# Optimization experiments

Hardware: AMD Instinct MI355X
Metric: run time of the kernel (lower is better)

The kernel has to match this reference:

```python
import jax, jax.numpy as jnp
import numpy as np

H = 128          # controller hidden size
NCELL = 8        # memory cells
CS = 8           # cell size
R = 1            # read heads
L = 16           # stacked DNC layers
E = 15           # embedding size
NCLS = 30
NUMFRI = 5
NN_IN = H + R * CS                   # 136, controller input width (layers > 0)
XI = R * CS + 3 * CS + 5 * R + 3     # 40, interface vector size
CLIP = 20.0
EPS = 1e-6
B, T = 128, 64
NOT_EYE = 1.0 - np.eye(NCELL, dtype=np.float32)


def setup_inputs() -> dict:
    key = jax.random.key(0)
    ks = iter(jax.random.split(key, 40))
    n = lambda shape, s=0.05: jax.random.normal(next(ks), shape, dtype=jnp.float32) * s
    return {
        "x": jax.random.randint(next(ks), (B, T), 0, NCLS, dtype=jnp.int32),
        "f": n((B, H * NUMFRI), 1.0),
        "embed": n((NCLS + 3, E), 1.0),
        # LSTM controller: [layer, sublayer(2), 4H, in] with in padded to NN_IN
        "W_ih": n((L, 2, 4 * H, NN_IN)),
        "W_hh": n((L, 2, 4 * H, H)),
        "b_ih": n((L, 2, 4 * H)),
        "b_hh": n((L, 2, 4 * H)),
        "W_if": n((XI, H)),            # memory interface
        "b_if": n((XI,)),
        "W_out": n((H, NN_IN)),        # final DNC output linear
        "b_out": n((H,)),
        "W_fri": n((H, H * NUMFRI)),
        "b_fri": n((H,)),
        "W_c1": n((H, 2 * H)),
        "b_c1": n((H,)),
        "W_c2": n((NCLS, H)),
        "b_c2": n((NCLS,)),
    }


def lstm_cell(x, h, c, wih, whh, bih, bhh):
    g = x @ wih.T + h @ whh.T + bih + bhh
    i, f, gg, o = jnp.split(g, 4, axis=-1)  # torch gate order i,f,g,o
    c2 = jax.nn.sigmoid(f) * c + jax.nn.sigmoid(i) * jnp.tanh(gg)
    h2 = jax.nn.sigmoid(o) * jnp.tanh(c2)
    return h2, c2


def content_weight(mem, keys, strengths):
    # cosine similarity between keys [b,h,cs] and memory rows [b,m,cs]
    mn = mem / (jnp.linalg.norm(mem, axis=2, keepdims=True) + EPS)
    kn = keys / (jnp.linalg.norm(keys, axis=2, keepdims=True) + EPS)
    sim = jnp.einsum('bhc,bmc->bhm', kn, mn)
    return jax.nn.softmax(sim * strengths[:, :, None], axis=2)


def allocate(usage):
    u = EPS + (1.0 - EPS) * usage
    phi = jnp.argsort(u, axis=1)          # free list (ascending usage)
    su = jnp.take_along_axis(u, phi, axis=1)
    shifted = jnp.cumprod(jnp.concatenate([jnp.ones_like(su[:, :1]), su], axis=1), axis=1)[:, :-1]
    sa = (1.0 - su) * shifted
    phi_rev = jnp.argsort(phi, axis=1)    # inverse permutation
    return jnp.take_along_axis(sa, phi_rev, axis=1)[:, None, :]   # [b,1,m]


def memory_step(xi, mstate):
    mem, link, prec, rw, ww, usage = mstate
    b = xi.shape[0]
    rk = jnp.tanh(xi[:, :R * CS].reshape(b, R, CS))
    rs = jax.nn.softplus(xi[:, R * CS:R * CS + R])
    wk = jnp.tanh(xi[:, R * CS + R:R * CS + R + CS].reshape(b, 1, CS))
    ws = jax.nn.softplus(xi[:, R * CS + R + CS:R * CS + R + CS + 1])
    er = jax.nn.sigmoid(xi[:, R * CS + R + CS + 1:R * CS + R + 2 * CS + 1].reshape(b, 1, CS))
    wv = jnp.tanh(xi[:, R * CS + R + 2 * CS + 1:R * CS + R + 3 * CS + 1].reshape(b, 1, CS))
    fg = jax.nn.sigmoid(xi[:, R * CS + R + 3 * CS + 1:R * CS + 2 * R + 3 * CS + 1])
    ag = jax.nn.sigmoid(xi[:, R * CS + 2 * R + 3 * CS + 1:R * CS + 2 * R + 3 * CS + 2])
    wg = jax.nn.sigmoid(xi[:, R * CS + 2 * R + 3 * CS + 2:R * CS + 2 * R + 3 * CS + 3])
    modes = jax.nn.softmax(xi[:, R * CS + 2 * R + 3 * CS + 3:].reshape(b, R, 3), axis=-1)
    # --- write ---
    usage = usage + (1 - usage) * (1 - jnp.prod(1 - ww, axis=1))
    psi = jnp.prod(1 - fg[:, :, None] * rw, axis=1)
    usage = usage * psi
    wcw = content_weight(mem, wk, ws)                  # [b,1,m]
    alloc = allocate(usage)
    a3 = ag[:, :, None]; g3 = wg[:, :, None]
    ww = g3 * (a3 * alloc + (1 - a3) * wcw)            # [b,1,m]
    reset = jnp.prod(1 - ww[:, :, :, None] * er[:, :, None, :], axis=1)  # [b,m,cs]
    mem = mem * reset + jnp.einsum('bhm,bhc->bmc', ww, wv)
    ww_i = ww[:, :, :, None]; ww_j = ww[:, :, None, :]
    link = (1 - ww_i - ww_j) * link + ww_i * prec[:, :, None, :]
    link = link * NOT_EYE[None, None]
    prec = (1 - jnp.sum(ww, axis=2, keepdims=True)) * prec + ww
    # --- read ---
    cw = content_weight(mem, rk, rs)                   # [b,r,m]
    fwdw = jnp.einsum('bhij,brj->brhi', link, rw)      # forward weightings
    bwdw = jnp.einsum('bri,bhij->brhj', rw, link)      # backward weightings
    rw = (modes[:, :, 2:3] * cw
          + jnp.sum(modes[:, :, 1:2][:, :, :, None] * fwdw, axis=2)
          + jnp.sum(modes[:, :, 0:1][:, :, :, None] * bwdw, axis=2))
    read_vecs = jnp.einsum('brm,bmc->brc', rw, mem).reshape(b, R * CS)
    return read_vecs, (mem, link, prec, rw, ww, usage)


def _forward(x, f, embed, W_ih, W_hh, b_ih, b_hh, W_if, b_if, W_out, b_out,
             W_fri, b_fri, W_c1, b_c1, W_c2, b_c2):
    b = x.shape[0]
    emb = embed[x]                                     # [b,t,E]
    carry0 = (jnp.zeros((L, 2, b, H), jnp.float32), jnp.zeros((L, 2, b, H), jnp.float32),
              jnp.zeros((b, NCELL, CS), jnp.float32), jnp.zeros((b, 1, NCELL, NCELL), jnp.float32),
              jnp.zeros((b, 1, NCELL), jnp.float32), jnp.zeros((b, R, NCELL), jnp.float32),
              jnp.zeros((b, 1, NCELL), jnp.float32), jnp.zeros((b, NCELL), jnp.float32))

    def step(carry, x_t):
        h, c, mem, link, prec, rw, ww, usage = carry
        inp = x_t   # layer-0 sees [x_t, zero initial read] (reset_experience=True); zeros come from padding
        hs, cs = [], []
        for l in range(L):
            xin = jnp.pad(inp, ((0, 0), (0, NN_IN - inp.shape[1])))
            h0, c0 = lstm_cell(xin, h[l, 0], c[l, 0], W_ih[l, 0], W_hh[l, 0], b_ih[l, 0], b_hh[l, 0])
            xin1 = jnp.pad(h0, ((0, 0), (0, NN_IN - H)))
            h1, c1 = lstm_cell(xin1, h[l, 1], c[l, 1], W_ih[l, 1], W_hh[l, 1], b_ih[l, 1], b_hh[l, 1])
            hs.append(jnp.stack([h0, h1])); cs.append(jnp.stack([c0, c1]))
            out = jnp.clip(h1, -CLIP, CLIP)
            xi = out @ W_if.T + b_if
            read_vecs, (mem, link, prec, rw, ww, usage) = memory_step(xi, (mem, link, prec, rw, ww, usage))
            inp = jnp.concatenate([out, read_vecs], axis=1)   # [b, 136] -> next layer
        y = inp @ W_out.T + b_out
        return (jnp.stack(hs), jnp.stack(cs), mem, link, prec, rw, ww, usage), y

    _, ys = jax.lax.scan(step, carry0, emb.transpose(1, 0, 2))
    z = ys[-1]                                         # encoder output = last timestep [b,H]
    f_out = jax.nn.relu(f @ W_fri.T + b_fri)
    hcat = jnp.concatenate([z, f_out], axis=1)         # [b,2H]
    h1 = jax.nn.relu(hcat @ W_c1.T + b_c1)
    return h1 @ W_c2.T + b_c2                          # [b, n_class]


def reference(x, f, embed, W_ih, W_hh, b_ih, b_hh, W_if, b_if, W_out, b_out,
              W_fri, b_fri, W_c1, b_c1, W_c2, b_c2):
    return _forward(x, f, embed, W_ih, W_hh, b_ih, b_hh, W_if, b_if, W_out, b_out,
                    W_fri, b_fri, W_c1, b_c1, W_c2, b_c2)
```

## Files before the change

### kernel.cpp

```cpp
#include <hip/hip_runtime.h>
#include <stdint.h>

#define LNUM 16
#define H 128
#define TT 64
#define NCLSN 30
#define EPSF 1e-6f

typedef _Float16 half2v __attribute__((ext_vector_type(2)));

__device__ inline float fdot2(uint32_t a, uint32_t b, float c) {
  return __builtin_amdgcn_fdot2(__builtin_bit_cast(half2v, a),
                                __builtin_bit_cast(half2v, b), c, false);
}
__device__ inline float dot8(uint4 w, uint4 xv, float a) {
  a = fdot2(w.x, xv.x, a); a = fdot2(w.y, xv.y, a);
  a = fdot2(w.z, xv.z, a); a = fdot2(w.w, xv.w, a);
  return a;
}
__device__ __forceinline__ float rcpf(float x) { return __builtin_amdgcn_rcpf(x); }
__device__ inline float sigf(float x) { return rcpf(1.0f + __expf(-x)); }
__device__ __forceinline__ float tanh_fast(float x) {
  float xc = fminf(fmaxf(x, -15.f), 15.f);
  float e = __expf(2.f * xc);
  return (e - 1.f) * rcpf(e + 1.f);
}
__device__ __forceinline__ float softplus_fast(float x) {
  return fmaxf(x, 0.f) + __logf(1.f + __expf(-fabsf(x)));
}
__device__ inline uint32_t packh2(float a, float b) {
  half2v h; h.x = (_Float16)a; h.y = (_Float16)b;
  return __builtin_bit_cast(uint32_t, h);
}
__device__ inline uint16_t f16bits(float a) {
  _Float16 h = (_Float16)a;
  return __builtin_bit_cast(uint16_t, h);
}
__device__ __forceinline__ void gl_lds16(const uint4* g, uint4* l) {
  __builtin_amdgcn_global_load_lds(
      (const __attribute__((address_space(1))) void*)g,
      (__attribute__((address_space(3))) void*)l, 16, 0, 0);
}
__device__ __forceinline__ void bar_lgkm() {
  asm volatile("s_waitcnt lgkmcnt(0)\ns_barrier" ::: "memory");
}

__global__ void prepA(const float* __restrict__ W_ih, const float* __restrict__ W_hh,
                      uint4* __restrict__ WB) {
  int idx = blockIdx.x * 256 + threadIdx.x;
  int lc = idx / 16896;
  int r  = idx % 16896;
  int row, kq;
  if (r < 16384) {
    int q = r >> 11;
    int rem = r & 2047;
    int g = rem >> 9;
    int gt = rem & 511;
    int j = gt >> 2, s = gt & 3;
    kq = s + 4 * q;
    row = g * 128 + j;
  } else {
    int r2 = r - 16384;
    int g = r2 >> 7, j = r2 & 127;
    kq = 32; row = g * 128 + j;
  }
  bool zero = ((lc & 1) && kq == 16);
  uint32_t p[4];
#pragma unroll
  for (int i2 = 0; i2 < 4; i2++) {
    float w0 = 0.f, w1 = 0.f;
    if (!zero) {
      int k0 = 8 * kq + 2 * i2;
      w0 = (k0 < 136) ? W_ih[((size_t)lc * 512 + row) * 136 + k0]
                      : W_hh[((size_t)lc * 512 + row) * 128 + (k0 - 136)];
      w1 = (k0 + 1 < 136) ? W_ih[((size_t)lc * 512 + row) * 136 + k0 + 1]
                          : W_hh[((size_t)lc * 512 + row) * 128 + (k0 + 1 - 136)];
    }
    p[i2] = packh2(w0, w1);
  }
  uint4 v; v.x = p[0]; v.y = p[1]; v.z = p[2]; v.w = p[3];
  WB[idx] = v;
}

__global__ void prepB(const float* __restrict__ b_ih, const float* __restrict__ b_hh,
                      const float* __restrict__ W_if, const float* __restrict__ W_fri,
                      const float* __restrict__ W_c1, const float* __restrict__ W_c2,
                      float* __restrict__ bias_comb, uint32_t* __restrict__ Wif16,
                      float* __restrict__ WfriT, float* __restrict__ Wc1T,
                      float* __restrict__ Wc2T) {
  int idx = blockIdx.x * 256 + threadIdx.x;
  if (idx < 16384) { bias_comb[idx] = b_ih[idx] + b_hh[idx]; return; }
  idx -= 16384;
  if (idx < 2560)  {
    int j = idx / 64, k2 = idx % 64;
    Wif16[idx] = packh2(W_if[j * 128 + 2 * k2], W_if[j * 128 + 2 * k2 + 1]);
    return;
  }
  idx -= 2560;
  if (idx < 81920) { int k = idx / 128, j = idx % 128; WfriT[idx] = W_fri[j * 640 + k]; return; }
  idx -= 81920;
  if (idx < 32768) { int k = idx / 128, j = idx % 128; Wc1T[idx]  = W_c1[j * 256 + k]; return; }
  idx -= 32768;
  if (idx < 3840)  { int k = idx / 30,  j = idx % 30;  Wc2T[idx]  = W_c2[j * 128 + k]; return; }
}

__device__ __forceinline__ void memstep_par(
    int m, const float* __restrict__ xi,
    float (&mm)[8], float (&lkr)[8],
    float& u, float& p, float& r, float& w,
    float (&rv)[8]) {
  float rk[8], wk[8], er[8], wv[8];
#pragma unroll
  for (int c = 0; c < 8; c++) {
    rk[c] = tanh_fast(xi[c]);
    wk[c] = tanh_fast(xi[9 + c]);
    er[c] = sigf(xi[18 + c]);
    wv[c] = tanh_fast(xi[26 + c]);
  }
  float rs  = softplus_fast(xi[8]);
  float wsd = softplus_fast(xi[17]);
  float fg  = sigf(xi[34]), ag = sigf(xi[35]), wg = sigf(xi[36]);
  float l0 = xi[37], l1 = xi[38], l2 = xi[39];
  float lmx = fmaxf(l0, fmaxf(l1, l2));
  float eb = __expf(l0 - lmx), ef = __expf(l1 - lmx), ec = __expf(l2 - lmx);
  float minv = rcpf(eb + ef + ec);
  float mode_b = eb * minv, mode_f = ef * minv, mode_c = ec * minv;

  u = u + (1.f - u) * w;
  u *= (1.f - fg * r);

  float kn2 = 0.f, mn2 = 0.f, dp = 0.f;
#pragma unroll
  for (int c = 0; c < 8; c++) { kn2 += wk[c]*wk[c]; mn2 += mm[c]*mm[c]; dp += wk[c]*mm[c]; }
  float sim = dp * rcpf((sqrtf(kn2) + EPSF) * (sqrtf(mn2) + EPSF)) * wsd;
  float mx = sim;
  mx = fmaxf(mx, __shfl_xor(mx, 1));
  mx = fmaxf(mx, __shfl_xor(mx, 2));
  mx = fmaxf(mx, __shfl_xor(mx, 4));
  float e = __expf(sim - mx);
  float se = e;
  se += __shfl_xor(se, 1); se += __shfl_xor(se, 2); se += __shfl_xor(se, 4);
  float wcw = e * rcpf(se);

  float up = EPSF + (1.f - EPSF) * u;
  float prod = 1.f;
#pragma unroll
  for (int n = 0; n < 8; n++) {
    float un = __shfl(up, n);
    bool before = (un < up) || (un == up && n < m);
    prod *= ((n != m) && before) ? un : 1.f;
  }
  float alloc = (1.f - up) * prod;
  float wn = wg * (ag * alloc + (1.f - ag) * wcw);
  float sw = wn;
  sw += __shfl_xor(sw, 1); sw += __shfl_xor(sw, 2); sw += __shfl_xor(sw, 4);

#pragma unroll
  for (int c = 0; c < 8; c++)
    mm[c] = mm[c] * (1.f - wn * er[c]) + wn * wv[c];

  float wnv[8], pvv[8];
#pragma unroll
  for (int n = 0; n < 8; n++) { wnv[n] = __shfl(wn, n); pvv[n] = __shfl(p, n); }
#pragma unroll
  for (int jj = 0; jj < 8; jj++)
    lkr[jj] = (jj == m) ? 0.f : ((1.f - wn - wnv[jj]) * lkr[jj] + wn * pvv[jj]);
  p = (1.f - sw) * p + wn;

  float rn2 = 0.f; mn2 = 0.f; dp = 0.f;
#pragma unroll
  for (int c = 0; c < 8; c++) { rn2 += rk[c]*rk[c]; mn2 += mm[c]*mm[c]; dp += rk[c]*mm[c]; }
  float sim2 = dp * rcpf((sqrtf(rn2) + EPSF) * (sqrtf(mn2) + EPSF)) * rs;
  float mx2 = sim2;
  mx2 = fmaxf(mx2, __shfl_xor(mx2, 1));
  mx2 = fmaxf(mx2, __shfl_xor(mx2, 2));
  mx2 = fmaxf(mx2, __shfl_xor(mx2, 4));
  float e2 = __expf(sim2 - mx2);
  float se2 = e2;
  se2 += __shfl_xor(se2, 1); se2 += __shfl_xor(se2, 2); se2 += __shfl_xor(se2, 4);
  float cw = e2 * rcpf(se2);

  float rv8[8];
#pragma unroll
  for (int n = 0; n < 8; n++) rv8[n] = __shfl(r, n);
  float fwd = 0.f;
#pragma unroll
  for (int jj = 0; jj < 8; jj++) fwd += lkr[jj] * rv8[jj];
  float bw[8];
#pragma unroll
  for (int jj = 0; jj < 8; jj++) bw[jj] = r * lkr[jj];
#pragma unroll
  for (int jj = 0; jj < 8; jj++) {
    bw[jj] += __shfl_xor(bw[jj], 1);
    bw[jj] += __shfl_xor(bw[jj], 2);
    bw[jj] += __shfl_xor(bw[jj], 4);
  }
  bool s1 = (m & 1) != 0, s2 = (m & 2) != 0, s4 = (m & 4) != 0;
  float t0 = s1 ? bw[1] : bw[0];
  float t1 = s1 ? bw[3] : bw[2];
  float t2 = s1 ? bw[5] : bw[4];
  float t3 = s1 ? bw[7] : bw[6];
  float q0 = s2 ? t1 : t0;
  float q1 = s2 ? t3 : t2;
  float bwd = s4 ? q1 : q0;

  float rn = mode_c * cw + mode_f * fwd + mode_b * bwd;

#pragma unroll
  for (int c = 0; c < 8; c++) rv[c] = rn * mm[c];
#pragma unroll
  for (int c = 0; c < 8; c++) {
    rv[c] += __shfl_xor(rv[c], 1);
    rv[c] += __shfl_xor(rv[c], 2);
    rv[c] += __shfl_xor(rv[c], 4);
  }
  r = rn; w = wn;
}

__device__ __forceinline__ void aux_work(
    int lane, bool write_inp,
    const uint4 (&wreg)[16], const float* __restrict__ b_if,
    const uint4* __restrict__ outhu4, float* __restrict__ xi_lds,
    uint4* __restrict__ inpu4,
    float (&mm)[8], float (&lkr)[8],
    float& u, float& p, float& r, float& w,
    float (&rv)[8]) {
  if (lane < 40) {
    float acc0 = 0.f, acc1 = 0.f;
#pragma unroll
    for (int q = 0; q < 8; q++) {
      acc0 = dot8(wreg[2 * q],     outhu4[2 * q],     acc0);
      acc1 = dot8(wreg[2 * q + 1], outhu4[2 * q + 1], acc1);
    }
    xi_lds[lane] = acc0 + acc1 + b_if[lane];
  }
  asm volatile("s_waitcnt lgkmcnt(0)" ::: "memory");
  __builtin_amdgcn_sched_barrier(0);
  __builtin_amdgcn_wave_barrier();
  if (lane < 8) {
    memstep_par(lane, xi_lds, mm, lkr, u, p, r, w, rv);
    if (write_inp && lane == 0) {
      uint4 pv4;
      pv4.x = packh2(rv[0], rv[1]); pv4.y = packh2(rv[2], rv[3]);
      pv4.z = packh2(rv[4], rv[5]); pv4.w = packh2(rv[6], rv[7]);
      inpu4[16] = pv4;
    }
  }
}

#define STAGE(lcX, qX, bbX)                                                    \
  do {                                                                         \
    const uint4* sp_ = WB + (size_t)(lcX) * 16896 + (size_t)(qX) * 2048 + tid; \
    uint4* dp_ = myslab + (size_t)(bbX) * 256;                                 \
    gl_lds16(sp_,        dp_);                                                 \
    gl_lds16(sp_ + 512,  dp_ + 64);                                            \
    gl_lds16(sp_ + 1024, dp_ + 128);                                           \
    gl_lds16(sp_ + 1536, dp_ + 192);                                           \
  } while (0)

__global__ __launch_bounds__(576) void dnc_main(
    const int* __restrict__ x, const float* __restrict__ embed,
    const uint4* __restrict__ WB, const float* __restrict__ bias_comb,
    const uint32_t* __restrict__ Wif16, const float* __restrict__ b_if,
    const float* __restrict__ W_out, const float* __restrict__ b_out,
    float* __restrict__ y_buf) {
  __shared__ __align__(16) uint16_t hst[32 * 128];
  __shared__ float c_st[32 * 128];
  __shared__ float emb_lds[495];
  __shared__ __align__(16) uint32_t inp16[17 * 4];
  __shared__ __align__(16) uint16_t outh16[128];
  __shared__ float inp_f32[128];
  __shared__ float xi_lds[40];
  __shared__ float rv_f32[8];
  __shared__ __align__(16) uint4 sbuf[8 * 4 * 256];

  uint4* inpu4 = (uint4*)inp16;
  uint4* hstu4 = (uint4*)hst;
  uint4* outhu4 = (uint4*)outh16;
  uint16_t* inpu16 = (uint16_t*)inp16;

  const int tid = threadIdx.x;
  const int b0 = blockIdx.x;
  const int ln = tid & 63;
  uint4* myslab = sbuf + (size_t)(tid >> 6) * 1024;

  float mm[8] = {0.f,0.f,0.f,0.f,0.f,0.f,0.f,0.f};
  float lkr[8] = {0.f,0.f,0.f,0.f,0.f,0.f,0.f,0.f};
  float p_u = 0.f, p_p = 0.f, p_r = 0.f, p_w = 0.f;
  float rvout[8];

  uint4 wreg[16];
  if (tid >= 512 && (tid & 63) < 40) {
    const uint4* wr = (const uint4*)(Wif16 + (tid & 63) * 64);
#pragma unroll
    for (int q = 0; q < 16; q++) wreg[q] = wr[q];
  }

  for (int i = tid; i < 32 * 128; i += 576) { hst[i] = 0; c_st[i] = 0.f; }
  for (int i = tid; i < 495; i += 576) emb_lds[i] = embed[i];
  __syncthreads();
  if (tid < 17) {
    int q = tid;
    int ix = x[b0 * TT + 0];
    uint32_t p0, p1, p2, p3;
    {
      int k0 = 8 * q;
      float e0 = (k0 < 15) ? emb_lds[ix * 15 + k0] : 0.f;
      float e1 = (k0 + 1 < 15) ? emb_lds[ix * 15 + k0 + 1] : 0.f;
      float e2 = (k0 + 2 < 15) ? emb_lds[ix * 15 + k0 + 2] : 0.f;
      float e3 = (k0 + 3 < 15) ? emb_lds[ix * 15 + k0 + 3] : 0.f;
      float e4 = (k0 + 4 < 15) ? emb_lds[ix * 15 + k0 + 4] : 0.f;
      float e5 = (k0 + 5 < 15) ? emb_lds[ix * 15 + k0 + 5] : 0.f;
      float e6 = (k0 + 6 < 15) ? emb_lds[ix * 15 + k0 + 6] : 0.f;
      float e7 = (k0 + 7 < 15) ? emb_lds[ix * 15 + k0 + 7] : 0.f;
      p0 = packh2(e0, e1); p1 = packh2(e2, e3); p2 = packh2(e4, e5); p3 = packh2(e6, e7);
    }
    uint4 v; v.x = p0; v.y = p1; v.z = p2; v.w = p3;
    inpu4[q] = v;
  }
  if (tid < 512) { STAGE(0, 0, 0); STAGE(0, 1, 1); STAGE(0, 2, 2); }
  __syncthreads();

  for (int t = 0; t < TT; ++t) {
    for (int l = 0; l < LNUM; ++l) {
      const int lc0 = l * 2, lc1 = l * 2 + 1;
      const int nlc0 = (l == 15) ? 0 : lc0 + 2;
      const int j = tid >> 2, s = tid & 3;
      float aA0 = 0.f, aA1 = 0.f, aA2 = 0.f, aA3 = 0.f;
      uint4 wd0 = {}, wd1 = {}, wd2 = {}, wd3 = {};
      float bA0 = 0.f, bA1 = 0.f, bA2 = 0.f, bA3 = 0.f;

      if (tid < 512) {
        uint4 wt0 = {}, wt1 = {}, wt2 = {}, wt3 = {};
        if (s == 0) {
          const uint4* wt = WB + (size_t)lc0 * 16896 + 16384 + j;
          wt0 = wt[0]; wt1 = wt[128]; wt2 = wt[256]; wt3 = wt[384];
        }
        if (s == 0) {
          const float* bb = bias_comb + lc0 * 512 + j;
          bA0 = bb[0]; bA1 = bb[128]; bA2 = bb[256]; bA3 = bb[384];
        }
#pragma unroll
        for (int q = 0; q < 8; q++) {
          if (q < 5) STAGE(lc0, q + 3, (q + 3) & 3);
          else       STAGE(lc1, q - 5, (q + 3) & 3);
          asm volatile("s_waitcnt vmcnt(12)" ::: "memory");
          __builtin_amdgcn_sched_barrier(0);
          const uint4* wb = myslab + (size_t)(q & 3) * 256 + ln;
          uint4 w0 = wb[0], w1 = wb[64], w2 = wb[128], w3 = wb[192];
          int kq = s + 4 * q;
          bool defer = (s == 0) && (q == 4);
          int kqe = defer ? 0 : kq;
          const uint4* xp = (kqe < 17) ? (inpu4 + kqe)
                                       : (hstu4 + lc0 * 16 + (kqe - 17));
          uint4 xv0 = *xp;
          if (defer) { wd0 = w0; wd1 = w1; wd2 = w2; wd3 = w3; }
          else {
            aA0 = dot8(w0, xv0, aA0);
            aA1 = dot8(w1, xv0, aA1);
            aA2 = dot8(w2, xv0, aA2);
            aA3 = dot8(w3, xv0, aA3);
          }
        }
        if (s == 0) {
          uint4 xv0 = hstu4[lc0 * 16 + 15];
          aA0 = dot8(wt0, xv0, aA0);
          aA1 = dot8(wt1, xv0, aA1);
          aA2 = dot8(wt2, xv0, aA2);
          aA3 = dot8(wt3, xv0, aA3);
        }
      } else if (t > 0 || l > 0) {
        const int lane = tid - 512;
        aux_work(lane, (l != 0), wreg, b_if, outhu4, xi_lds,
                 inpu4, mm, lkr, p_u, p_p, p_r, p_w, rvout);
      }
      bar_lgkm();

      if (tid < 512) {
        if (s == 0) {
          uint4 xr0 = inpu4[16];
          aA0 = dot8(wd0, xr0, aA0);
          aA1 = dot8(wd1, xr0, aA1);
          aA2 = dot8(wd2, xr0, aA2);
          aA3 = dot8(wd3, xr0, aA3);
        }
        aA0 += __shfl_xor(aA0, 1); aA0 += __shfl_xor(aA0, 2);
        aA1 += __shfl_xor(aA1, 1); aA1 += __shfl_xor(aA1, 2);
        aA2 += __shfl_xor(aA2, 1); aA2 += __shfl_xor(aA2, 2);
        aA3 += __shfl_xor(aA3, 1); aA3 += __shfl_xor(aA3, 2);
        if (s == 0) {
          float gi = aA0 + bA0, gf = aA1 + bA1, gg = aA2 + bA2, go = aA3 + bA3;
          int ci = lc0 * 128 + j;
          float c2 = sigf(gf) * c_st[ci] + sigf(gi) * tanh_fast(gg);
          c_st[ci] = c2;
          hst[ci] = f16bits(sigf(go) * tanh_fast(c2));
        }
      }
      bar_lgkm();

      if (tid < 512) {
        float cA0 = 0.f, cA1 = 0.f, cA2 = 0.f, cA3 = 0.f;
        uint4 wt0 = {}, wt1 = {}, wt2 = {}, wt3 = {};
        float bC0 = 0.f, bC1 = 0.f, bC2 = 0.f, bC3 = 0.f;
        if (s == 0) {
          const uint4* wt = WB + (size_t)lc1 * 16896 + 16384 + j;
          wt0 = wt[0]; wt1 = wt[128]; wt2 = wt[256]; wt3 = wt[384];
          const float* bb = bias_comb + lc1 * 512 + j;
          bC0 = bb[0]; bC1 = bb[128]; bC2 = bb[256]; bC3 = bb[384];
        }
#pragma unroll
        for (int q = 0; q < 8; q++) {
          if (q < 5) STAGE(lc1, q + 3, (q + 3) & 3);
          else       STAGE(nlc0, q - 5, (q + 3) & 3);
          asm volatile("s_waitcnt vmcnt(12)" ::: "memory");
          __builtin_amdgcn_sched_barrier(0);
          const uint4* wb = myslab + (size_t)(q & 3) * 256 + ln;
          uint4 w0 = wb[0], w1 = wb[64], w2 = wb[128], w3 = wb[192];
          int kq = s + 4 * q;
          const uint4* xp = (kq < 17) ? (hstu4 + lc0 * 16 + kq)
                                      : (hstu4 + lc1 * 16 + (kq - 17));
          uint4 xv0 = *xp;
          cA0 = dot8(w0, xv0, cA0);
          cA1 = dot8(w1, xv0, cA1);
          cA2 = dot8(w2, xv0, cA2);
          cA3 = dot8(w3, xv0, cA3);
        }
        if (s == 0) {
          uint4 xv0 = hstu4[lc1 * 16 + 15];
          cA0 = dot8(wt0, xv0, cA0);
          cA1 = dot8(wt1, xv0, cA1);
          cA2 = dot8(wt2, xv0, cA2);
          cA3 = dot8(wt3, xv0, cA3);
        }
        cA0 += __shfl_xor(cA0, 1); cA0 += __shfl_xor(cA0, 2);
        cA1 += __shfl_xor(cA1, 1); cA1 += __shfl_xor(cA1, 2);
        cA2 += __shfl_xor(cA2, 1); cA2 += __shfl_xor(cA2, 2);
        cA3 += __shfl_xor(cA3, 1); cA3 += __shfl_xor(cA3, 2);
        if (s == 0) {
          float gi = cA0 + bC0, gf = cA1 + bC1, gg = cA2 + bC2, go = cA3 + bC3;
          int ci = lc1 * 128 + j;
          float c2 = sigf(gf) * c_st[ci] + sigf(gi) * tanh_fast(gg);
          c_st[ci] = c2;
          float h2 = sigf(go) * tanh_fast(c2);
          hst[ci] = f16bits(h2);
          inp_f32[j] = h2;
          outh16[j] = f16bits(h2);
          if (l != 15) inpu16[j] = f16bits(h2);
        }
      } else {
        const int lane = tid - 512;
        if (l == 15 && t < 63 && lane < 17) {
          int q = lane;
          int ix = x[b0 * TT + t + 1];
          uint32_t p0, p1, p2, p3;
          {
            int k0 = 8 * q;
            float e0 = (k0 < 15) ? emb_lds[ix * 15 + k0] : 0.f;
            float e1 = (k0 + 1 < 15) ? emb_lds[ix * 15 + k0 + 1] : 0.f;
            float e2 = (k0 + 2 < 15) ? emb_lds[ix * 15 + k0 + 2] : 0.f;
            float e3 = (k0 + 3 < 15) ? emb_lds[ix * 15 + k0 + 3] : 0.f;
            float e4 = (k0 + 4 < 15) ? emb_lds[ix * 15 + k0 + 4] : 0.f;
            float e5 = (k0 + 5 < 15) ? emb_lds[ix * 15 + k0 + 5] : 0.f;
            float e6 = (k0 + 6 < 15) ? emb_lds[ix * 15 + k0 + 6] : 0.f;
            float e7 = (k0 + 7 < 15) ? emb_lds[ix * 15 + k0 + 7] : 0.f;
            p0 = packh2(e0, e1); p1 = packh2(e2, e3); p2 = packh2(e4, e5); p3 = packh2(e6, e7);
          }
          uint4 v; v.x = p0; v.y = p1; v.z = p2; v.w = p3;
          inpu4[q] = v;
        }
      }
      bar_lgkm();
    }
  }

  if (tid >= 512) {
    const int lane = tid - 512;
    aux_work(lane, false, wreg, b_if, outhu4, xi_lds,
             inpu4, mm, lkr, p_u, p_p, p_r, p_w, rvout);
    if (lane == 0) {
#pragma unroll
      for (int c = 0; c < 8; c++) rv_f32[c] = rvout[c];
    }
  }
  __syncthreads();
  if (tid < 128) {
    int i = tid;
    float a = b_out[i];
    for (int k = 0; k < 128; ++k) a += inp_f32[k] * W_out[i * 136 + k];
    for (int k = 0; k < 8; ++k)   a += rv_f32[k] * W_out[i * 136 + 128 + k];
    y_buf[b0 * H + i] = a;
  }
}

__global__ void head_kernel(const float* __restrict__ y_buf, const float* __restrict__ f,
                            const float* __restrict__ WfriT, const float* __restrict__ b_fri,
                            const float* __restrict__ Wc1T, const float* __restrict__ b_c1,
                            const float* __restrict__ Wc2T, const float* __restrict__ b_c2,
                            float* __restrict__ out) {
  __shared__ float fl[640], yl[128], fo[128], h1l[128];
  int b = blockIdx.x, j = threadIdx.x;
  for (int i = j; i < 640; i += 128) fl[i] = f[b * 640 + i];
  yl[j] = y_buf[b * 128 + j];
  __syncthreads();
  float a = b_fri[j];
  for (int k = 0; k < 640; ++k) a += fl[k] * WfriT[k * 128 + j];
  fo[j] = fmaxf(a, 0.f);
  __syncthreads();
  float a2 = b_c1[j];
  for (int k = 0; k < 128; ++k) a2 += yl[k] * Wc1T[k * 128 + j];
  for (int k = 0; k < 128; ++k) a2 += fo[k] * Wc1T[(128 + k) * 128 + j];
  h1l[j] = fmaxf(a2, 0.f);
  __syncthreads();
  if (j < NCLSN) {
    float a3 = b_c2[j];
    for (int k = 0; k < 128; ++k) a3 += h1l[k] * Wc2T[k * NCLSN + j];
    out[b * NCLSN + j] = a3;
  }
}

extern "C" void kernel_launch(void* const* d_in, const int* in_sizes, int n_in,
                              void* d_out, int out_size, void* d_ws, size_t ws_size,
                              hipStream_t stream) {
  const int*   x     = (const int*)d_in[0];
  const float* f     = (const float*)d_in[1];
  const float* embed = (const float*)d_in[2];
  const float* W_ih  = (const float*)d_in[3];
  const float* W_hh  = (const float*)d_in[4];
  const float* b_ih  = (const float*)d_in[5];
  const float* b_hh  = (const float*)d_in[6];
  const float* W_if  = (const float*)d_in[7];
  const float* b_if  = (const float*)d_in[8];
  const float* W_out = (const float*)d_in[9];
  const float* b_out = (const float*)d_in[10];
  const float* W_fri = (const float*)d_in[11];
  const float* b_fri = (const float*)d_in[12];
  const float* W_c1  = (const float*)d_in[13];
  const float* b_c1  = (const float*)d_in[14];
  const float* W_c2  = (const float*)d_in[15];
  const float* b_c2  = (const float*)d_in[16];

  uint8_t* ws = (uint8_t*)d_ws;
  uint4* WB        = (uint4*)(ws + 0);
  float* bias_comb = (float*)(ws + 8650752);
  uint32_t* Wif16  = (uint32_t*)(ws + 8716288);
  float* WfriT     = (float*)(ws + 8726528);
  float* Wc1T      = (float*)(ws + 9054208);
  float* Wc2T      = (float*)(ws + 9185280);
  float* y_buf     = (float*)(ws + 9200640);
  float* out       = (float*)d_out;

  prepA<<<2112, 256, 0, stream>>>(W_ih, W_hh, WB);
  prepB<<<537, 256, 0, stream>>>(b_ih, b_hh, W_if, W_fri, W_c1, W_c2,
                                 bias_comb, Wif16, WfriT, Wc1T, Wc2T);
  dnc_main<<<128, 576, 0, stream>>>(x, embed, WB, bias_comb, Wif16, b_if,
                                    W_out, b_out, y_buf);
  head_kernel<<<128, 128, 0, stream>>>(y_buf, f, WfriT, b_fri, Wc1T, b_c1,
                                       Wc2T, b_c2, out);
}
```

Before: 10.03 ms.

## Repartition LSTM gate matvec across 16 waves with row-pair split and deeper weight ring

Raises the main recurrent kernel from 576 to 1024 threads. Gate rows are now split across 14 gate waves, with two lanes per row streaming weights through an 8-slot LDS ring. A 15th wave reads its last 64 rows straight from global, and the 16th wave runs the memory/interface work. Biases are folded into the packed weights as an extra column dotted with a constant one, and the interface weights move from registers to LDS. The gate nonlinearity is computed by 128 threads from a shared gates buffer. This adds an extra barrier per sublayer in exchange for more parallelism and fewer serial dot products per thread.

```diff
diff --git a/kernel.cpp b/kernel.cpp
--- a/kernel.cpp
+++ b/kernel.cpp
@@ -2,10 +2,10 @@
 #include <stdint.h>
 
 #define LNUM 16
-#define H 128
 #define TT 64
 #define NCLSN 30
 #define EPSF 1e-6f
+#define NBUF 8
 
 typedef _Float16 half2v __attribute__((ext_vector_type(2)));
 
@@ -45,52 +45,76 @@
   asm volatile("s_waitcnt lgkmcnt(0)\ns_barrier" ::: "memory");
 }
 
-__global__ void prepA(const float* __restrict__ W_ih, const float* __restrict__ W_hh,
-                      uint4* __restrict__ WB) {
+__global__ void prepWR(const float* __restrict__ W_ih, const float* __restrict__ W_hh,
+                       const float* __restrict__ b_ih, const float* __restrict__ b_hh,
+                       uint4* __restrict__ WR) {
   int idx = blockIdx.x * 256 + threadIdx.x;
-  int lc = idx / 16896;
-  int r  = idx % 16896;
-  int row, kq;
-  if (r < 16384) {
-    int q = r >> 11;
-    int rem = r & 2047;
-    int g = rem >> 9;
-    int gt = rem & 511;
-    int j = gt >> 2, s = gt & 3;
-    kq = s + 4 * q;
-    row = g * 128 + j;
+  if (idx >= 487424) return;
+  int tid = idx % 896;
+  int rem = idx / 896;
+  int i = rem % 17;
+  int lc = rem / 17;
+  int r = tid >> 1, s = tid & 1;
+  uint32_t p0 = 0, p1 = 0, p2 = 0, p3 = 0;
+  if (s == 1 && i == 16) {
+    float b = b_ih[(size_t)lc * 512 + r] + b_hh[(size_t)lc * 512 + r];
+    p0 = packh2(b, 0.f);
   } else {
-    int r2 = r - 16384;
-    int g = r2 >> 7, j = r2 & 127;
-    kq = 32; row = g * 128 + j;
-  }
-  bool zero = ((lc & 1) && kq == 16);
-  uint32_t p[4];
-#pragma unroll
-  for (int i2 = 0; i2 < 4; i2++) {
-    float w0 = 0.f, w1 = 0.f;
+    int c = s ? 17 + i : i;
+    bool zero = ((lc & 1) != 0) && (c == 16);
     if (!zero) {
-      int k0 = 8 * kq + 2 * i2;
-      w0 = (k0 < 136) ? W_ih[((size_t)lc * 512 + row) * 136 + k0]
-                      : W_hh[((size_t)lc * 512 + row) * 128 + (k0 - 136)];
-      w1 = (k0 + 1 < 136) ? W_ih[((size_t)lc * 512 + row) * 136 + k0 + 1]
-                          : W_hh[((size_t)lc * 512 + row) * 128 + (k0 + 1 - 136)];
-    }
-    p[i2] = packh2(w0, w1);
-  }
-  uint4 v; v.x = p[0]; v.y = p[1]; v.z = p[2]; v.w = p[3];
-  WB[idx] = v;
-}
-
-__global__ void prepB(const float* __restrict__ b_ih, const float* __restrict__ b_hh,
-                      const float* __restrict__ W_if, const float* __restrict__ W_fri,
+      float w[8];
+#pragma unroll
+      for (int e = 0; e < 8; e++) {
+        int k = 8 * c + e;
+        w[e] = (k < 136) ? W_ih[((size_t)lc * 512 + r) * 136 + k]
+                         : W_hh[((size_t)lc * 512 + r) * 128 + (k - 136)];
+      }
+      p0 = packh2(w[0], w[1]); p1 = packh2(w[2], w[3]);
+      p2 = packh2(w[4], w[5]); p3 = packh2(w[6], w[7]);
+    }
+  }
+  uint4 v; v.x = p0; v.y = p1; v.z = p2; v.w = p3;
+  WR[idx] = v;
+}
+
+__global__ void prepWC(const float* __restrict__ W_ih, const float* __restrict__ W_hh,
+                       const float* __restrict__ b_ih, const float* __restrict__ b_hh,
+                       uint4* __restrict__ WC) {
+  int idx = blockIdx.x * 256 + threadIdx.x;
+  if (idx >= 69632) return;
+  int k = idx % 64;
+  int rem = idx / 64;
+  int c = rem % 34;
+  int lc = rem / 34;
+  int r = 448 + k;
+  uint32_t p0 = 0, p1 = 0, p2 = 0, p3 = 0;
+  if (c == 33) {
+    float b = b_ih[(size_t)lc * 512 + r] + b_hh[(size_t)lc * 512 + r];
+    p0 = packh2(b, 0.f);
+  } else {
+    bool zero = ((lc & 1) != 0) && (c == 16);
+    if (!zero) {
+      float w[8];
+#pragma unroll
+      for (int e = 0; e < 8; e++) {
+        int kk = 8 * c + e;
+        w[e] = (kk < 136) ? W_ih[((size_t)lc * 512 + r) * 136 + kk]
+                          : W_hh[((size_t)lc * 512 + r) * 128 + (kk - 136)];
+      }
+      p0 = packh2(w[0], w[1]); p1 = packh2(w[2], w[3]);
+      p2 = packh2(w[4], w[5]); p3 = packh2(w[6], w[7]);
+    }
+  }
+  uint4 v; v.x = p0; v.y = p1; v.z = p2; v.w = p3;
+  WC[idx] = v;
+}
+
+__global__ void prepB(const float* __restrict__ W_if, const float* __restrict__ W_fri,
                       const float* __restrict__ W_c1, const float* __restrict__ W_c2,
-                      float* __restrict__ bias_comb, uint32_t* __restrict__ Wif16,
-                      float* __restrict__ WfriT, float* __restrict__ Wc1T,
-                      float* __restrict__ Wc2T) {
+                      uint32_t* __restrict__ Wif16, float* __restrict__ WfriT,
+                      float* __restrict__ Wc1T, float* __restrict__ Wc2T) {
   int idx = blockIdx.x * 256 + threadIdx.x;
-  if (idx < 16384) { bias_comb[idx] = b_ih[idx] + b_hh[idx]; return; }
-  idx -= 16384;
   if (idx < 2560)  {
     int j = idx / 64, k2 = idx % 64;
     Wif16[idx] = packh2(W_if[j * 128 + 2 * k2], W_if[j * 128 + 2 * k2 + 1]);
@@ -218,8 +242,8 @@
 }
 
 __device__ __forceinline__ void aux_work(
-    int lane, bool write_inp,
-    const uint4 (&wreg)[16], const float* __restrict__ b_if,
+    int lane, bool write_inp, float bifr,
+    const uint4* __restrict__ wifu4,
     const uint4* __restrict__ outhu4, float* __restrict__ xi_lds,
     uint4* __restrict__ inpu4,
     float (&mm)[8], float (&lkr)[8],
@@ -227,12 +251,13 @@
     float (&rv)[8]) {
   if (lane < 40) {
     float acc0 = 0.f, acc1 = 0.f;
+    const uint4* wr = wifu4 + lane * 16;
 #pragma unroll
     for (int q = 0; q < 8; q++) {
-      acc0 = dot8(wreg[2 * q],     outhu4[2 * q],     acc0);
-      acc1 = dot8(wreg[2 * q + 1], outhu4[2 * q + 1], acc1);
-    }
-    xi_lds[lane] = acc0 + acc1 + b_if[lane];
+      acc0 = dot8(wr[2 * q],     outhu4[2 * q],     acc0);
+      acc1 = dot8(wr[2 * q + 1], outhu4[2 * q + 1], acc1);
+    }
+    xi_lds[lane] = acc0 + acc1 + bifr;
   }
   asm volatile("s_waitcnt lgkmcnt(0)" ::: "memory");
   __builtin_amdgcn_sched_barrier(0);
@@ -248,235 +273,209 @@
   }
 }
 
-#define STAGE(lcX, qX, bbX)                                                    \
-  do {                                                                         \
-    const uint4* sp_ = WB + (size_t)(lcX) * 16896 + (size_t)(qX) * 2048 + tid; \
-    uint4* dp_ = myslab + (size_t)(bbX) * 256;                                 \
-    gl_lds16(sp_,        dp_);                                                 \
-    gl_lds16(sp_ + 512,  dp_ + 64);                                            \
-    gl_lds16(sp_ + 1024, dp_ + 128);                                           \
-    gl_lds16(sp_ + 1536, dp_ + 192);                                           \
-  } while (0)
-
-__global__ __launch_bounds__(576) void dnc_main(
+__global__ __launch_bounds__(1024) void dnc_main(
     const int* __restrict__ x, const float* __restrict__ embed,
-    const uint4* __restrict__ WB, const float* __restrict__ bias_comb,
+    const uint4* __restrict__ WR, const uint4* __restrict__ WC,
     const uint32_t* __restrict__ Wif16, const float* __restrict__ b_if,
     const float* __restrict__ W_out, const float* __restrict__ b_out,
     float* __restrict__ y_buf) {
   __shared__ __align__(16) uint16_t hst[32 * 128];
   __shared__ float c_st[32 * 128];
+  __shared__ float gates_lds[512];
+  __shared__ __align__(16) uint32_t wif_lds[2560];
   __shared__ float emb_lds[495];
   __shared__ __align__(16) uint32_t inp16[17 * 4];
   __shared__ __align__(16) uint16_t outh16[128];
   __shared__ float inp_f32[128];
   __shared__ float xi_lds[40];
   __shared__ float rv_f32[8];
-  __shared__ __align__(16) uint4 sbuf[8 * 4 * 256];
+  __shared__ __align__(16) uint4 one1v;
+  __shared__ __align__(16) uint4 sbuf[14 * NBUF * 64];
 
   uint4* inpu4 = (uint4*)inp16;
   uint4* hstu4 = (uint4*)hst;
   uint4* outhu4 = (uint4*)outh16;
   uint16_t* inpu16 = (uint16_t*)inp16;
+  const uint4* wifu4 = (const uint4*)wif_lds;
 
   const int tid = threadIdx.x;
   const int b0 = blockIdx.x;
-  const int ln = tid & 63;
-  uint4* myslab = sbuf + (size_t)(tid >> 6) * 1024;
+  const int wave = tid >> 6, lane = tid & 63;
+  const bool isGW  = (wave < 14);
+  const bool isW14 = (wave == 14);
+  const int r = tid >> 1, s = tid & 1;
+  uint4* myslab = sbuf + (size_t)wave * (NBUF * 64);
 
   float mm[8] = {0.f,0.f,0.f,0.f,0.f,0.f,0.f,0.f};
   float lkr[8] = {0.f,0.f,0.f,0.f,0.f,0.f,0.f,0.f};
   float p_u = 0.f, p_p = 0.f, p_r = 0.f, p_w = 0.f;
   float rvout[8];
-
-  uint4 wreg[16];
-  if (tid >= 512 && (tid & 63) < 40) {
-    const uint4* wr = (const uint4*)(Wif16 + (tid & 63) * 64);
-#pragma unroll
-    for (int q = 0; q < 16; q++) wreg[q] = wr[q];
-  }
-
-  for (int i = tid; i < 32 * 128; i += 576) { hst[i] = 0; c_st[i] = 0.f; }
-  for (int i = tid; i < 495; i += 576) emb_lds[i] = embed[i];
+  float bifr = 0.f;
+  if (wave == 15 && lane < 40) bifr = b_if[lane];
+
+  for (int i = tid; i < 32 * 128; i += 1024) { hst[i] = 0; c_st[i] = 0.f; }
+  for (int i = tid; i < 2560; i += 1024) wif_lds[i] = Wif16[i];
+  for (int i = tid; i < 495; i += 1024) emb_lds[i] = embed[i];
+  if (tid == 0) { uint4 v; v.x = packh2(1.f, 0.f); v.y = 0; v.z = 0; v.w = 0; one1v = v; }
   __syncthreads();
   if (tid < 17) {
     int q = tid;
     int ix = x[b0 * TT + 0];
-    uint32_t p0, p1, p2, p3;
-    {
-      int k0 = 8 * q;
-      float e0 = (k0 < 15) ? emb_lds[ix * 15 + k0] : 0.f;
-      float e1 = (k0 + 1 < 15) ? emb_lds[ix * 15 + k0 + 1] : 0.f;
-      float e2 = (k0 + 2 < 15) ? emb_lds[ix * 15 + k0 + 2] : 0.f;
-      float e3 = (k0 + 3 < 15) ? emb_lds[ix * 15 + k0 + 3] : 0.f;
-      float e4 = (k0 + 4 < 15) ? emb_lds[ix * 15 + k0 + 4] : 0.f;
-      float e5 = (k0 + 5 < 15) ? emb_lds[ix * 15 + k0 + 5] : 0.f;
-      float e6 = (k0 + 6 < 15) ? emb_lds[ix * 15 + k0 + 6] : 0.f;
-      float e7 = (k0 + 7 < 15) ? emb_lds[ix * 15 + k0 + 7] : 0.f;
-      p0 = packh2(e0, e1); p1 = packh2(e2, e3); p2 = packh2(e4, e5); p3 = packh2(e6, e7);
-    }
-    uint4 v; v.x = p0; v.y = p1; v.z = p2; v.w = p3;
+    uint32_t e[8];
+#pragma unroll
+    for (int e2 = 0; e2 < 8; e2++) {
+      int k0 = 8 * q + e2;
+      ((float*)e)[e2] = (k0 < 15) ? emb_lds[ix * 15 + k0] : 0.f;
+    }
+    float* ef = (float*)e;
+    uint4 v;
+    v.x = packh2(ef[0], ef[1]); v.y = packh2(ef[2], ef[3]);
+    v.z = packh2(ef[4], ef[5]); v.w = packh2(ef[6], ef[7]);
     inpu4[q] = v;
   }
-  if (tid < 512) { STAGE(0, 0, 0); STAGE(0, 1, 1); STAGE(0, 2, 2); }
   __syncthreads();
+
+  int base = 0;
+  if (isGW) {
+#pragma unroll
+    for (int p5 = 0; p5 < 7; p5++)
+      gl_lds16(WR + (size_t)p5 * 896 + tid, myslab + (size_t)p5 * 64);
+  }
 
   for (int t = 0; t < TT; ++t) {
     for (int l = 0; l < LNUM; ++l) {
       const int lc0 = l * 2, lc1 = l * 2 + 1;
       const int nlc0 = (l == 15) ? 0 : lc0 + 2;
-      const int j = tid >> 2, s = tid & 3;
-      float aA0 = 0.f, aA1 = 0.f, aA2 = 0.f, aA3 = 0.f;
-      uint4 wd0 = {}, wd1 = {}, wd2 = {}, wd3 = {};
-      float bA0 = 0.f, bA1 = 0.f, bA2 = 0.f, bA3 = 0.f;
-
-      if (tid < 512) {
-        uint4 wt0 = {}, wt1 = {}, wt2 = {}, wt3 = {};
-        if (s == 0) {
-          const uint4* wt = WB + (size_t)lc0 * 16896 + 16384 + j;
-          wt0 = wt[0]; wt1 = wt[128]; wt2 = wt[256]; wt3 = wt[384];
+      float acc = 0.f;
+      uint4 wd = {};
+
+      if (isGW) {
+#pragma unroll
+        for (int q = 0; q < 17; q++) {
+          asm volatile("s_waitcnt vmcnt(6)" ::: "memory");
+          __builtin_amdgcn_sched_barrier(0);
+          uint4 w = myslab[(size_t)((base + q) & 7) * 64 + lane];
+          uint4 xv;
+          if (s == 0) xv = (q < 16) ? inpu4[q] : inpu4[16];
+          else        xv = (q < 16) ? hstu4[lc0 * 16 + q] : one1v;
+          if (s == 0 && q == 16) wd = w;
+          else acc = dot8(w, xv, acc);
+          const int pp = q + 7;
+          const uint4* src = (pp <= 16)
+              ? WR + ((size_t)lc0 * 17 + pp) * 896 + tid
+              : WR + ((size_t)lc1 * 17 + (pp - 17)) * 896 + tid;
+          gl_lds16(src, myslab + (size_t)((base + pp) & 7) * 64);
         }
-        if (s == 0) {
-          const float* bb = bias_comb + lc0 * 512 + j;
-          bA0 = bb[0]; bA1 = bb[128]; bA2 = bb[256]; bA3 = bb[384];
-        }
-#pragma unroll
-        for (int q = 0; q < 8; q++) {
-          if (q < 5) STAGE(lc0, q + 3, (q + 3) & 3);
-          else       STAGE(lc1, q - 5, (q + 3) & 3);
-          asm volatile("s_waitcnt vmcnt(12)" ::: "memory");
-          __builtin_amdgcn_sched_barrier(0);
-          const uint4* wb = myslab + (size_t)(q & 3) * 256 + ln;
-          uint4 w0 = wb[0], w1 = wb[64], w2 = wb[128], w3 = wb[192];
-          int kq = s + 4 * q;
-          bool defer = (s == 0) && (q == 4);
-          int kqe = defer ? 0 : kq;
-          const uint4* xp = (kqe < 17) ? (inpu4 + kqe)
-                                       : (hstu4 + lc0 * 16 + (kqe - 17));
-          uint4 xv0 = *xp;
-          if (defer) { wd0 = w0; wd1 = w1; wd2 = w2; wd3 = w3; }
-          else {
-            aA0 = dot8(w0, xv0, aA0);
-            aA1 = dot8(w1, xv0, aA1);
-            aA2 = dot8(w2, xv0, aA2);
-            aA3 = dot8(w3, xv0, aA3);
-          }
-        }
-        if (s == 0) {
-          uint4 xv0 = hstu4[lc0 * 16 + 15];
-          aA0 = dot8(wt0, xv0, aA0);
-          aA1 = dot8(wt1, xv0, aA1);
-          aA2 = dot8(wt2, xv0, aA2);
-          aA3 = dot8(wt3, xv0, aA3);
-        }
-      } else if (t > 0 || l > 0) {
-        const int lane = tid - 512;
-        aux_work(lane, (l != 0), wreg, b_if, outhu4, xi_lds,
-                 inpu4, mm, lkr, p_u, p_p, p_r, p_w, rvout);
-      }
-      bar_lgkm();
-
-      if (tid < 512) {
-        if (s == 0) {
-          uint4 xr0 = inpu4[16];
-          aA0 = dot8(wd0, xr0, aA0);
-          aA1 = dot8(wd1, xr0, aA1);
-          aA2 = dot8(wd2, xr0, aA2);
-          aA3 = dot8(wd3, xr0, aA3);
-        }
-        aA0 += __shfl_xor(aA0, 1); aA0 += __shfl_xor(aA0, 2);
-        aA1 += __shfl_xor(aA1, 1); aA1 += __shfl_xor(aA1, 2);
-        aA2 += __shfl_xor(aA2, 1); aA2 += __shfl_xor(aA2, 2);
-        aA3 += __shfl_xor(aA3, 1); aA3 += __shfl_xor(aA3, 2);
-        if (s == 0) {
-          float gi = aA0 + bA0, gf = aA1 + bA1, gg = aA2 + bA2, go = aA3 + bA3;
-          int ci = lc0 * 128 + j;
-          float c2 = sigf(gf) * c_st[ci] + sigf(gi) * tanh_fast(gg);
-          c_st[ci] = c2;
-          hst[ci] = f16bits(sigf(go) * tanh_fast(c2));
-        }
-      }
-      bar_lgkm();
-
-      if (tid < 512) {
-        float cA0 = 0.f, cA1 = 0.f, cA2 = 0.f, cA3 = 0.f;
-        uint4 wt0 = {}, wt1 = {}, wt2 = {}, wt3 = {};
-        float bC0 = 0.f, bC1 = 0.f, bC2 = 0.f, bC3 = 0.f;
-        if (s == 0) {
-          const uint4* wt = WB + (size_t)lc1 * 16896 + 16384 + j;
-          wt0 = wt[0]; wt1 = wt[128]; wt2 = wt[256]; wt3 = wt[384];
-          const float* bb = bias_comb + lc1 * 512 + j;
-          bC0 = bb[0]; bC1 = bb[128]; bC2 = bb[256]; bC3 = bb[384];
-        }
-#pragma unroll
-        for (int q = 0; q < 8; q++) {
-          if (q < 5) STAGE(lc1, q + 3, (q + 3) & 3);
-          else       STAGE(nlc0, q - 5, (q + 3) & 3);
-          asm volatile("s_waitcnt vmcnt(12)" ::: "memory");
-          __builtin_amdgcn_sched_barrier(0);
-          const uint4* wb = myslab + (size_t)(q & 3) * 256 + ln;
-          uint4 w0 = wb[0], w1 = wb[64], w2 = wb[128], w3 = wb[192];
-          int kq = s + 4 * q;
-          const uint4* xp = (kq < 17) ? (hstu4 + lc0 * 16 + kq)
-                                      : (hstu4 + lc1 * 16 + (kq - 17));
-          uint4 xv0 = *xp;
-          cA0 = dot8(w0, xv0, cA0);
-          cA1 = dot8(w1, xv0, cA1);
-          cA2 = dot8(w2, xv0, cA2);
-          cA3 = dot8(w3, xv0, cA3);
-        }
-        if (s == 0) {
-          uint4 xv0 = hstu4[lc1 * 16 + 15];
-          cA0 = dot8(wt0, xv0, cA0);
-          cA1 = dot8(wt1, xv0, cA1);
-          cA2 = dot8(wt2, xv0, cA2);
-          cA3 = dot8(wt3, xv0, cA3);
-        }
-        cA0 += __shfl_xor(cA0, 1); cA0 += __shfl_xor(cA0, 2);
-        cA1 += __shfl_xor(cA1, 1); cA1 += __shfl_xor(cA1, 2);
-        cA2 += __shfl_xor(cA2, 1); cA2 += __shfl_xor(cA2, 2);
-        cA3 += __shfl_xor(cA3, 1); cA3 += __shfl_xor(cA3, 2);
-        if (s == 0) {
-          float gi = cA0 + bC0, gf = cA1 + bC1, gg = cA2 + bC2, go = cA3 + bC3;
-          int ci = lc1 * 128 + j;
-          float c2 = sigf(gf) * c_st[ci] + sigf(gi) * tanh_fast(gg);
-          c_st[ci] = c2;
-          float h2 = sigf(go) * tanh_fast(c2);
-          hst[ci] = f16bits(h2);
-          inp_f32[j] = h2;
-          outh16[j] = f16bits(h2);
-          if (l != 15) inpu16[j] = f16bits(h2);
+      } else if (isW14) {
+        const uint4* wc = WC + (size_t)lc0 * 34 * 64 + lane;
+#pragma unroll
+        for (int c = 0; c < 34; c++) {
+          uint4 w = wc[c * 64];
+          if (c == 16) { wd = w; continue; }
+          uint4 xv;
+          if (c < 16)      xv = inpu4[c];
+          else if (c < 33) xv = hstu4[lc0 * 16 + (c - 17)];
+          else             xv = one1v;
+          acc = dot8(w, xv, acc);
         }
       } else {
-        const int lane = tid - 512;
+        if (t > 0 || l > 0)
+          aux_work(lane, (l != 0), bifr, wifu4, outhu4,
+                   xi_lds, inpu4, mm, lkr, p_u, p_p, p_r, p_w, rvout);
+      }
+      base = (base + 17) & 7;
+      bar_lgkm();
+
+      if (isGW) {
+        if (s == 0) acc = dot8(wd, inpu4[16], acc);
+        acc += __shfl_xor(acc, 1);
+        if (s == 0) gates_lds[r] = acc;
+      } else if (isW14) {
+        acc = dot8(wd, inpu4[16], acc);
+        gates_lds[448 + lane] = acc;
+      }
+      bar_lgkm();
+
+      if (tid < 128) {
+        float gi = gates_lds[tid], gf = gates_lds[128 + tid];
+        float gg = gates_lds[256 + tid], go = gates_lds[384 + tid];
+        int ci = lc0 * 128 + tid;
+        float c2 = sigf(gf) * c_st[ci] + sigf(gi) * tanh_fast(gg);
+        c_st[ci] = c2;
+        hst[ci] = f16bits(sigf(go) * tanh_fast(c2));
+      }
+      bar_lgkm();
+
+      float cacc = 0.f;
+      if (isGW) {
+#pragma unroll
+        for (int q = 0; q < 17; q++) {
+          asm volatile("s_waitcnt vmcnt(6)" ::: "memory");
+          __builtin_amdgcn_sched_barrier(0);
+          uint4 w = myslab[(size_t)((base + q) & 7) * 64 + lane];
+          uint4 xv;
+          if (s == 0) xv = (q < 16) ? hstu4[lc0 * 16 + q] : one1v;
+          else        xv = (q < 16) ? hstu4[lc1 * 16 + q] : one1v;
+          cacc = dot8(w, xv, cacc);
+          const int pp = q + 7;
+          const uint4* src = (pp <= 16)
+              ? WR + ((size_t)lc1 * 17 + pp) * 896 + tid
+              : WR + ((size_t)nlc0 * 17 + (pp - 17)) * 896 + tid;
+          gl_lds16(src, myslab + (size_t)((base + pp) & 7) * 64);
+        }
+        cacc += __shfl_xor(cacc, 1);
+        if (s == 0) gates_lds[r] = cacc;
+      } else if (isW14) {
+        const uint4* wc = WC + (size_t)lc1 * 34 * 64 + lane;
+#pragma unroll
+        for (int c = 0; c < 34; c++) {
+          uint4 w = wc[c * 64];
+          uint4 xv;
+          if (c < 16)       xv = hstu4[lc0 * 16 + c];
+          else if (c == 16) xv = one1v;
+          else if (c < 33)  xv = hstu4[lc1 * 16 + (c - 17)];
+          else              xv = one1v;
+          cacc = dot8(w, xv, cacc);
+        }
+        gates_lds[448 + lane] = cacc;
+      } else {
         if (l == 15 && t < 63 && lane < 17) {
           int q = lane;
           int ix = x[b0 * TT + t + 1];
-          uint32_t p0, p1, p2, p3;
-          {
-            int k0 = 8 * q;
-            float e0 = (k0 < 15) ? emb_lds[ix * 15 + k0] : 0.f;
-            float e1 = (k0 + 1 < 15) ? emb_lds[ix * 15 + k0 + 1] : 0.f;
-            float e2 = (k0 + 2 < 15) ? emb_lds[ix * 15 + k0 + 2] : 0.f;
-            float e3 = (k0 + 3 < 15) ? emb_lds[ix * 15 + k0 + 3] : 0.f;
-            float e4 = (k0 + 4 < 15) ? emb_lds[ix * 15 + k0 + 4] : 0.f;
-            float e5 = (k0 + 5 < 15) ? emb_lds[ix * 15 + k0 + 5] : 0.f;
-            float e6 = (k0 + 6 < 15) ? emb_lds[ix * 15 + k0 + 6] : 0.f;
-            float e7 = (k0 + 7 < 15) ? emb_lds[ix * 15 + k0 + 7] : 0.f;
-            p0 = packh2(e0, e1); p1 = packh2(e2, e3); p2 = packh2(e4, e5); p3 = packh2(e6, e7);
+          float ef[8];
+#pragma unroll
+          for (int e2 = 0; e2 < 8; e2++) {
+            int k0 = 8 * q + e2;
+            ef[e2] = (k0 < 15) ? emb_lds[ix * 15 + k0] : 0.f;
           }
-          uint4 v; v.x = p0; v.y = p1; v.z = p2; v.w = p3;
+          uint4 v;
+          v.x = packh2(ef[0], ef[1]); v.y = packh2(ef[2], ef[3]);
+          v.z = packh2(ef[4], ef[5]); v.w = packh2(ef[6], ef[7]);
           inpu4[q] = v;
         }
       }
+      base = (base + 17) & 7;
       bar_lgkm();
-    }
-  }
-
-  if (tid >= 512) {
-    const int lane = tid - 512;
-    aux_work(lane, false, wreg, b_if, outhu4, xi_lds,
-             inpu4, mm, lkr, p_u, p_p, p_r, p_w, rvout);
+
+      if (tid < 128) {
+        float gi = gates_lds[tid], gf = gates_lds[128 + tid];
+        float gg = gates_lds[256 + tid], go = gates_lds[384 + tid];
+        int ci = lc1 * 128 + tid;
+        float c2 = sigf(gf) * c_st[ci] + sigf(gi) * tanh_fast(gg);
+        c_st[ci] = c2;
+        float h2 = sigf(go) * tanh_fast(c2);
+        hst[ci] = f16bits(h2);
+        inp_f32[tid] = h2;
+        outh16[tid] = f16bits(h2);
+        if (l != 15) inpu16[tid] = f16bits(h2);
+      }
+      bar_lgkm();
+    }
+  }
+
+  if (wave == 15) {
+    aux_work(lane, false, bifr, wifu4, outhu4,
+             xi_lds, inpu4, mm, lkr, p_u, p_p, p_r, p_w, rvout);
     if (lane == 0) {
 #pragma unroll
       for (int c = 0; c < 8; c++) rv_f32[c] = rvout[c];
@@ -488,7 +487,7 @@
     float a = b_out[i];
     for (int k = 0; k < 128; ++k) a += inp_f32[k] * W_out[i * 136 + k];
     for (int k = 0; k < 8; ++k)   a += rv_f32[k] * W_out[i * 136 + 128 + k];
-    y_buf[b0 * H + i] = a;
+    y_buf[b0 * 128 + i] = a;
   }
 }
 
@@ -540,20 +539,20 @@
   const float* b_c2  = (const float*)d_in[16];
 
   uint8_t* ws = (uint8_t*)d_ws;
-  uint4* WB        = (uint4*)(ws + 0);
-  float* bias_comb = (float*)(ws + 8650752);
-  uint32_t* Wif16  = (uint32_t*)(ws + 8716288);
-  float* WfriT     = (float*)(ws + 8726528);
-  float* Wc1T      = (float*)(ws + 9054208);
-  float* Wc2T      = (float*)(ws + 9185280);
-  float* y_buf     = (float*)(ws + 9200640);
+  uint4* WR        = (uint4*)(ws + 0);
+  uint4* WC        = (uint4*)(ws + 7798784);
+  uint32_t* Wif16  = (uint32_t*)(ws + 8912896);
+  float* WfriT     = (float*)(ws + 8923136);
+  float* Wc1T      = (float*)(ws + 9250816);
+  float* Wc2T      = (float*)(ws + 9381888);
+  float* y_buf     = (float*)(ws + 9397248);
   float* out       = (float*)d_out;
 
-  prepA<<<2112, 256, 0, stream>>>(W_ih, W_hh, WB);
-  prepB<<<537, 256, 0, stream>>>(b_ih, b_hh, W_if, W_fri, W_c1, W_c2,
-                                 bias_comb, Wif16, WfriT, Wc1T, Wc2T);
-  dnc_main<<<128, 576, 0, stream>>>(x, embed, WB, bias_comb, Wif16, b_if,
-                                    W_out, b_out, y_buf);
+  prepWR<<<1904, 256, 0, stream>>>(W_ih, W_hh, b_ih, b_hh, WR);
+  prepWC<<<272, 256, 0, stream>>>(W_ih, W_hh, b_ih, b_hh, WC);
+  prepB<<<473, 256, 0, stream>>>(W_if, W_fri, W_c1, W_c2, Wif16, WfriT, Wc1T, Wc2T);
+  dnc_main<<<128, 1024, 0, stream>>>(x, embed, WR, WC, Wif16, b_if,
+                                     W_out, b_out, y_buf);
   head_kernel<<<128, 128, 0, stream>>>(y_buf, f, WfriT, b_fri, Wc1T, b_c1,
                                        Wc2T, b_c2, out);
 }
```

Measured after the change: 17.75 ms. +77.1%, slower.
